# Kernel optimization log

Hardware: AMD Instinct MI355X
Metric: run time of the kernel (lower is better)

Reference implementation:

```python
import jax, jax.numpy as jnp
import numpy as np

B, K, H, W = 16, 32, 28, 28   # batch, set size, image h, image w
HID, OUT = 64, 64             # hid_dim, out_dim
NOPS = 8                      # permutation-equivariant 3->3 pool/broadcast basis ops


def setup_inputs() -> dict:
    key = jax.random.key(0)
    ks = jax.random.split(key, 8)
    def p(k, shape, fan_in):
        return jax.random.normal(k, shape, jnp.float32) / np.float32(np.sqrt(fan_in))
    return dict(
        x=jax.random.normal(ks[0], (B, K, H, W), jnp.float32),
        conv1_w=p(ks[1], (32, 1, 3, 3), 9),
        conv1_b=jnp.zeros((32,), jnp.float32),
        conv2_w=p(ks[2], (64, 32, 3, 3), 32 * 9),
        conv2_b=jnp.zeros((64,), jnp.float32),
        fc_w=p(ks[3], (HID, 64 * 7 * 7), 64 * 7 * 7),
        fc_b=jnp.zeros((HID,), jnp.float32),
        eq_w=p(ks[4], (HID, OUT, NOPS), HID * NOPS),
        eq_b=jnp.zeros((OUT,), jnp.float32),
        out_w=p(ks[5], (1, OUT), OUT),
        out_b=jnp.zeros((1,), jnp.float32),
    )


def _conv2d(x, w, b):
    y = jax.lax.conv_general_dilated(x, w, (1, 1), 'SAME',
                                     dimension_numbers=('NCHW', 'OIHW', 'NCHW'))
    return y + b[None, :, None, None]


def _maxpool2(x):
    return jax.lax.reduce_window(x, -jnp.inf, jax.lax.max,
                                 (1, 1, 2, 2), (1, 1, 2, 2), 'VALID')


def _forward(x, conv1_w, conv1_b, conv2_w, conv2_b, fc_w, fc_b, eq_w, eq_b, out_w, out_b):
    # --- BasicConvNet embed: (B*K, 1, H, W) -> (B*K, HID) ---
    x1 = x.reshape(B * K, 1, H, W)
    h1 = _maxpool2(jax.nn.relu(_conv2d(x1, conv1_w, conv1_b)))   # (B*K, 32, 14, 14)
    h2 = _maxpool2(jax.nn.relu(_conv2d(h1, conv2_w, conv2_b)))   # (B*K, 64, 7, 7)
    feat = jax.nn.relu(h2.reshape(B * K, -1) @ fc_w.T + fc_b)    # (B*K, HID)
    x4 = feat.reshape(B, K, HID)

    # --- triple outer product: (B, HID, K, K, K), no contracted index ---
    x5 = jnp.einsum('bid,bjd,bkd->bdijk', x4, x4, x4)

    # --- SetEq3to3: 8 equivariant pool/broadcast basis ops, contracted with eq_w[d,e,o].
    # Contract each pooled tensor with its slice of eq_w BEFORE broadcasting (same math,
    # avoids materializing 8 full (B,d,K,K,K) op tensors). ---
    m_i  = x5.mean(2)           # (B, d, j, k)
    m_j  = x5.mean(3)           # (B, d, i, k)
    m_k  = x5.mean(4)           # (B, d, i, j)
    m_ij = m_i.mean(2)          # (B, d, k)
    m_ik = m_i.mean(3)          # (B, d, j)
    m_jk = m_j.mean(3)          # (B, d, i)
    m_all = m_ij.mean(2)        # (B, d)

    x6 = (jnp.einsum('bdijk,de->beijk', x5, eq_w[:, :, 0])
          + jnp.einsum('bdjk,de->bejk', m_i, eq_w[:, :, 1])[:, :, None, :, :]
          + jnp.einsum('bdik,de->beik', m_j, eq_w[:, :, 2])[:, :, :, None, :]
          + jnp.einsum('bdij,de->beij', m_k, eq_w[:, :, 3])[:, :, :, :, None]
          + jnp.einsum('bdk,de->bek', m_ij, eq_w[:, :, 4])[:, :, None, None, :]
          + jnp.einsum('bdj,de->bej', m_ik, eq_w[:, :, 5])[:, :, None, :, None]
          + jnp.einsum('bdi,de->bei', m_jk, eq_w[:, :, 6])[:, :, :, None, None]
          + jnp.einsum('bd,de->be', m_all, eq_w[:, :, 7])[:, :, None, None, None]
          + eq_b[None, :, None, None, None])          # (B, OUT, K, K, K)

    # permute to channels-last, relu, pool over (i,j,k), relu, final linear
    x7 = jax.nn.relu(x6.transpose(0, 2, 3, 4, 1))     # (B, K, K, K, OUT)
    x8 = x7.mean(axis=(1, 2, 3))                      # (B, OUT)
    x9 = jax.nn.relu(x8)
    # dropout_prob = 0 -> identity
    return x9 @ out_w.T + out_b                       # (B, 1)


def reference(x, conv1_w, conv1_b, conv2_w, conv2_b, fc_w, fc_b, eq_w, eq_b, out_w, out_b):
    return _forward(x, conv1_w, conv1_b, conv2_w, conv2_b, fc_w, fc_b,
                    eq_w, eq_b, out_w, out_b)
```

## Files before the change

kernel.cpp:

```cpp
#include <hip/hip_runtime.h>
#include <hip/hip_bf16.h>


typedef __attribute__((ext_vector_type(8))) short short8;
typedef __attribute__((ext_vector_type(4))) float f32x4;

__device__ __forceinline__ f32x4 mfma_bf16(short8 a, short8 b, f32x4 c) {
  return __builtin_amdgcn_mfma_f32_16x16x32_bf16(a, b, c, 0, 0, 0);
}

__device__ __forceinline__ unsigned short f2bs(float f) {
  unsigned int u = __float_as_uint(f);
  unsigned int r = u + 0x7fffu + ((u >> 16) & 1u);
  return (unsigned short)(r >> 16);
}
__device__ __forceinline__ unsigned int pk2(float x, float y) {
  union { __hip_bfloat162 h; unsigned int u; } cv;
  cv.h = __float22bfloat162_rn(make_float2(x, y));
  return cv.u;
}
__device__ __forceinline__ void ub8(const short* p, float* f) {
  uint4 u = *(const uint4*)p;
  f[0] = __uint_as_float(u.x << 16); f[1] = __uint_as_float(u.x & 0xffff0000u);
  f[2] = __uint_as_float(u.y << 16); f[3] = __uint_as_float(u.y & 0xffff0000u);
  f[4] = __uint_as_float(u.z << 16); f[5] = __uint_as_float(u.z & 0xffff0000u);
  f[6] = __uint_as_float(u.w << 16); f[7] = __uint_as_float(u.w & 0xffff0000u);
}

__global__ __launch_bounds__(256) void k0_prep(const float* __restrict__ eqw,
    const float* __restrict__ w2, const float* __restrict__ fcw,
    float* __restrict__ W7t, short* __restrict__ Wtb,
    short* __restrict__ w2p, short* __restrict__ fcwb) {
  const int b = blockIdx.x, t = threadIdx.x;
  if (b < 8) {
    const int m = b;
    for (int idx = t; idx < 4096; idx += 256) {
      int e = idx >> 6, d = idx & 63;
      float v = eqw[d*512 + e*8 + m];
      if (m == 7) W7t[idx] = v;
      else        Wtb[m*4096 + idx] = (short)f2bs(v);
    }
  } else if (b == 8) {
    for (int idx = t; idx < 18432; idx += 256) {
      int s2 = idx & 7, c = (idx >> 3) & 63, quad = (idx >> 9) & 3, dd = idx >> 11;
      w2p[idx] = (short)f2bs(w2[c*288 + (quad*8 + s2)*9 + dd]);
    }
  } else {
    int base = (b - 9)*12544 + t;
    for (int q = 0; q < 49; ++q) {
      int idx = base + q*256;
      fcwb[idx] = (short)f2bs(fcw[idx]);
    }
  }
}

__global__ __launch_bounds__(256, 2) void kA_conv(const float* __restrict__ x,
    const float* __restrict__ w1, const float* __restrict__ b1,
    const short* __restrict__ w2p, const float* __restrict__ b2,
    const short* __restrict__ fcwb, const float* __restrict__ fcb,
    float* __restrict__ feat) {
  const int n = blockIdx.x, t = threadIdx.x;
  __shared__ float si[30*30];
  __shared__ float sw[32*9];
  __shared__ float sb[32];
  __shared__ __align__(16) short inT[16*18*40];
  __shared__ __align__(16) float h2f[3136];
  __shared__ float sf4[256];
  const int wv = t >> 6, l = t & 63, quad = l >> 4, col = l & 15;

  const int c_out = wv*16 + col;
  short8 Bq[9];
  {
    const short8* wp = (const short8*)w2p + quad*64 + c_out;
#pragma unroll
    for (int dd = 0; dd < 9; ++dd) Bq[dd] = wp[dd*256];
  }
  const float bb2 = b2[c_out];

  for (int idx = t; idx < 900; idx += 256) si[idx] = 0.f;
  {
    unsigned int* zp = (unsigned int*)inT;
    for (int idx = t; idx < 5760; idx += 256) zp[idx] = 0u;
  }
  for (int idx = t; idx < 288; idx += 256) sw[idx] = w1[idx];
  if (t < 32) sb[t] = b1[t];
  __syncthreads();
  for (int idx = t; idx < 784; idx += 256) {
    int y = idx / 28, xx = idx - y*28;
    si[(y+1)*30 + xx + 1] = x[n*784 + idx];
  }
  __syncthreads();

  {
    const int cg = t & 7;
    float wreg[4][9], breg[4];
#pragma unroll
    for (int cc = 0; cc < 4; ++cc) {
      breg[cc] = sb[cg*4 + cc];
#pragma unroll
      for (int q = 0; q < 9; ++q) wreg[cc][q] = sw[(cg*4 + cc)*9 + q];
    }
    for (int idx = t; idx < 1568; idx += 256) {
      int pos = idx >> 3;
      int py = pos / 14, px = pos - py*14;
      float pt[4][4];
#pragma unroll
      for (int r = 0; r < 4; ++r)
#pragma unroll
        for (int q = 0; q < 4; ++q)
          pt[r][q] = si[(2*py + r)*30 + 2*px + q];
      float res[4];
#pragma unroll
      for (int cc = 0; cc < 4; ++cc) {
        float best = 0.f;
#pragma unroll
        for (int a = 0; a < 2; ++a)
#pragma unroll
          for (int b3 = 0; b3 < 2; ++b3) {
            float v = breg[cc]
              + wreg[cc][0]*pt[a+0][b3+0] + wreg[cc][1]*pt[a+0][b3+1] + wreg[cc][2]*pt[a+0][b3+2]
              + wreg[cc][3]*pt[a+1][b3+0] + wreg[cc][4]*pt[a+1][b3+1] + wreg[cc][5]*pt[a+1][b3+2]
              + wreg[cc][6]*pt[a+2][b3+0] + wreg[cc][7]*pt[a+2][b3+1] + wreg[cc][8]*pt[a+2][b3+2];
            best = fmaxf(best, v);
          }
        res[cc] = best;
      }
      uint2 pkd;
      pkd.x = pk2(res[0], res[1]);
      pkd.y = pk2(res[2], res[3]);
      *(uint2*)&inT[(py+1)*720 + (px+1)*40 + cg*4] = pkd;
    }
  }
  __syncthreads();

  for (int p = 0; p < 7; ++p) {
    short8 Ar[4][3];
#pragma unroll
    for (int rr = 0; rr < 4; ++rr)
#pragma unroll
      for (int dx = 0; dx < 3; ++dx)
        Ar[rr][dx] = *(const short8*)&inT[(2*p + rr)*720 + (col + dx)*40 + quad*8];
    f32x4 a0 = {0.f,0.f,0.f,0.f}, a1 = {0.f,0.f,0.f,0.f};
#pragma unroll
    for (int dy = 0; dy < 3; ++dy)
#pragma unroll
      for (int dx = 0; dx < 3; ++dx) {
        a0 = mfma_bf16(Ar[dy][dx],     Bq[dy*3 + dx], a0);
        a1 = mfma_bf16(Ar[dy + 1][dx], Bq[dy*3 + dx], a1);
      }
#pragma unroll
    for (int a = 0; a < 2; ++a) {
      int px = quad*2 + a;
      if (px < 7) {
        float m0 = fmaxf(fmaxf(a0[2*a], a0[2*a + 1]), fmaxf(a1[2*a], a1[2*a + 1]));
        h2f[c_out*49 + p*7 + px] = fmaxf(m0 + bb2, 0.f);
      }
    }
  }
  {
    const short* Wrow = fcwb + l*3136 + wv*784;
    const float* Hrow = h2f + wv*784;
    float a0 = 0.f, a1 = 0.f, a2 = 0.f, a3 = 0.f;
#pragma unroll 7
    for (int j = 0; j < 98; ++j) {
      float wf[8]; ub8(&Wrow[j*8], wf);
      float4 hx = *(const float4*)&Hrow[j*8];
      float4 hy = *(const float4*)&Hrow[j*8 + 4];
      a0 += wf[0]*hx.x + wf[4]*hy.x;
      a1 += wf[1]*hx.y + wf[5]*hy.y;
      a2 += wf[2]*hx.z + wf[6]*hy.z;
      a3 += wf[3]*hx.w + wf[7]*hy.w;
    }
    sf4[wv*64 + l] = (a0 + a1) + (a2 + a3);
  }
  __syncthreads();
  if (t < 64) {
    float v = sf4[t] + sf4[64 + t] + sf4[128 + t] + sf4[192 + t] + fcb[t];
    feat[n*64 + t] = fmaxf(v, 0.f);
  }
}

__global__ __launch_bounds__(256) void k5_mfma(const float* __restrict__ feat,
    const short* __restrict__ Wtb, const float* __restrict__ W7t,
    const float* __restrict__ eqb, float* __restrict__ x8p) {
  __shared__ __align__(16) float Fm[32*68];
  __shared__ __align__(16) float FI[64];
  __shared__ __align__(16) float SV[64];
  __shared__ __align__(16) float SC[64];
  __shared__ __align__(16) float TC[64];
  __shared__ __align__(16) float C0[64];
  __shared__ float C0P[128];
  __shared__ float KCf[32*68];
  __shared__ float JCf[32*68];
  __shared__ float RED[256];
  __shared__ __align__(16) short Fb[32*72];
  __shared__ __align__(16) short QPb[64*72];
  __shared__ __align__(16) short G2b[64*72];
  __shared__ __align__(16) short G3b[64*72];

  const int i = blockIdx.x, b = blockIdx.y, t = threadIdx.x;
  const int w = t >> 6, l = t & 63, quad = l >> 4, col = l & 15;

  for (int idx = t; idx < 2048; idx += 256) {
    int r = idx >> 6, d = idx & 63;
    float v = feat[b*2048 + idx];
    Fm[r*68 + d] = v;
    Fb[r*72 + d] = (short)f2bs(v);
  }
  if (t < 64) FI[t] = feat[b*2048 + i*64 + t];
  __syncthreads();

  if (t < 64) {
    float a = 0.f;
#pragma unroll
    for (int r = 0; r < 32; ++r) a += Fm[r*68 + t];
    a *= (1.f/32.f);
    SV[t] = a;
    SC[t] = a*a*a;
  }
  __syncthreads();

  if (t < 64) {
    const float* W7 = W7t + t*64;
    float acc = 0.f;
#pragma unroll
    for (int d = 0; d < 64; d += 4) {
      float4 w4 = *(const float4*)&W7[d];
      acc += SC[d]*w4.x + SC[d+1]*w4.y + SC[d+2]*w4.z + SC[d+3]*w4.w;
    }
    TC[t] = acc + eqb[t];
  }

  {
    const int e = t >> 2, dbase = (t & 3) * 16;
#pragma unroll
    for (int h = 0; h < 2; ++h) {
      int off = dbase + h*8;
      float w0[8], w1r[8], w2r[8], w3r[8], w4r[8], w5r[8];
      ub8(&Wtb[0*4096 + e*64 + off], w0);
      ub8(&Wtb[1*4096 + e*64 + off], w1r);
      ub8(&Wtb[2*4096 + e*64 + off], w2r);
      ub8(&Wtb[3*4096 + e*64 + off], w3r);
      ub8(&Wtb[4*4096 + e*64 + off], w4r);
      ub8(&Wtb[5*4096 + e*64 + off], w5r);
      uint4 qv, g2v, g3v;
      unsigned int* qp = &qv.x;
      unsigned int* g2p = &g2v.x;
      unsigned int* g3p = &g3v.x;
#pragma unroll
      for (int j = 0; j < 4; ++j) {
        float fi0 = FI[off + 2*j],     fi1 = FI[off + 2*j + 1];
        float s0  = SV[off + 2*j],     s1  = SV[off + 2*j + 1];
        float q0 = fi0*w0[2*j]   + s0*w1r[2*j];
        float q1 = fi1*w0[2*j+1] + s1*w1r[2*j+1];
        float a0 = s0*(fi0*w2r[2*j]   + s0*w4r[2*j]);
        float a1 = s1*(fi1*w2r[2*j+1] + s1*w4r[2*j+1]);
        float c0 = s0*(fi0*w3r[2*j]   + s0*w5r[2*j]);
        float c1 = s1*(fi1*w3r[2*j+1] + s1*w5r[2*j+1]);
        qp[j]  = pk2(q0, q1);
        g2p[j] = pk2(a0, a1);
        g3p[j] = pk2(c0, c1);
      }
      *(uint4*)&QPb[e*72 + off] = qv;
      *(uint4*)&G2b[e*72 + off] = g2v;
      *(uint4*)&G3b[e*72 + off] = g3v;
    }
  }
  if (t < 128) {
    int e = t & 63, dh = t >> 6;
    const short* W6 = Wtb + 6*4096 + e*64 + dh*32;
    float a = 0.f;
#pragma unroll
    for (int g = 0; g < 4; ++g) {
      float wf[8];
      ub8(&W6[g*8], wf);
#pragma unroll
      for (int dd = 0; dd < 8; ++dd) {
        int d = dh*32 + g*8 + dd;
        float sd = SV[d];
        a += sd*sd*FI[d]*wf[dd];
      }
    }
    C0P[dh*64 + e] = a;
  }
  __syncthreads();

  if (w < 2) {
    const short* G = w ? G3b : G2b;
    float* DST = w ? JCf : KCf;
    short8 Bf[4][2];
#pragma unroll
    for (int n = 0; n < 4; ++n)
#pragma unroll
      for (int s2 = 0; s2 < 2; ++s2)
        Bf[n][s2] = *(const short8*)&G[(n*16 + col)*72 + s2*32 + quad*8];
#pragma unroll
    for (int m = 0; m < 2; ++m) {
      short8 A0 = *(const short8*)&Fb[(m*16 + col)*72 + quad*8];
      short8 A1 = *(const short8*)&Fb[(m*16 + col)*72 + 32 + quad*8];
#pragma unroll
      for (int n = 0; n < 4; ++n) {
        f32x4 z = {0.f, 0.f, 0.f, 0.f};
        f32x4 ac = mfma_bf16(A1, Bf[n][1], mfma_bf16(A0, Bf[n][0], z));
#pragma unroll
        for (int r = 0; r < 4; ++r)
          DST[(m*16 + quad*4 + r)*68 + n*16 + col] = ac[r];
      }
    }
  } else if (w == 2) {
    C0[l] = C0P[l] + C0P[64 + l] + TC[l];
  }
  __syncthreads();

  float kcv[2][4][4];
#pragma unroll
  for (int kb2 = 0; kb2 < 2; ++kb2)
#pragma unroll
    for (int r = 0; r < 4; ++r)
#pragma unroll
      for (int n = 0; n < 4; ++n)
        kcv[kb2][r][n] = KCf[(kb2*16 + quad*4 + r)*68 + n*16 + col];
  short8 Bq[4][2];
#pragma unroll
  for (int n = 0; n < 4; ++n)
#pragma unroll
    for (int s2 = 0; s2 < 2; ++s2)
      Bq[n][s2] = *(const short8*)&QPb[(n*16 + col)*72 + s2*32 + quad*8];

  float4 fkv[2][4];
#pragma unroll
  for (int kb2 = 0; kb2 < 2; ++kb2) {
    const float* fk = &Fm[(kb2*16 + col)*68 + quad*8];
    fkv[kb2][0] = *(const float4*)(fk);
    fkv[kb2][1] = *(const float4*)(fk + 4);
    fkv[kb2][2] = *(const float4*)(fk + 32);
    fkv[kb2][3] = *(const float4*)(fk + 36);
  }

  float sum[4] = {0.f, 0.f, 0.f, 0.f};
  union SU { short8 v; unsigned int u[4]; };

#pragma unroll
  for (int jj = 0; jj < 8; ++jj) {
    float jcq[4];
#pragma unroll
    for (int n = 0; n < 4; ++n)
      jcq[n] = JCf[(w*8 + jj)*68 + n*16 + col] + C0[n*16 + col];
    const float* fj = &Fm[(w*8 + jj)*68 + quad*8];
    float4 j0 = *(const float4*)(fj);
    float4 j1 = *(const float4*)(fj + 4);
    float4 j2 = *(const float4*)(fj + 32);
    float4 j3 = *(const float4*)(fj + 36);
#pragma unroll
    for (int kb2 = 0; kb2 < 2; ++kb2) {
      float4 k0 = fkv[kb2][0], k1 = fkv[kb2][1];
      float4 k2v = fkv[kb2][2], k3v = fkv[kb2][3];
      SU A0, A1;
      A0.u[0] = pk2(j0.x*k0.x, j0.y*k0.y);
      A0.u[1] = pk2(j0.z*k0.z, j0.w*k0.w);
      A0.u[2] = pk2(j1.x*k1.x, j1.y*k1.y);
      A0.u[3] = pk2(j1.z*k1.z, j1.w*k1.w);
      A1.u[0] = pk2(j2.x*k2v.x, j2.y*k2v.y);
      A1.u[1] = pk2(j2.z*k2v.z, j2.w*k2v.w);
      A1.u[2] = pk2(j3.x*k3v.x, j3.y*k3v.y);
      A1.u[3] = pk2(j3.z*k3v.z, j3.w*k3v.w);
      f32x4 ac[4];
#pragma unroll
      for (int n = 0; n < 4; ++n) {
        f32x4 z = {0.f, 0.f, 0.f, 0.f};
        ac[n] = mfma_bf16(A1.v, Bq[n][1], mfma_bf16(A0.v, Bq[n][0], z));
      }
#pragma unroll
      for (int n = 0; n < 4; ++n)
#pragma unroll
        for (int r = 0; r < 4; ++r) {
          float v = ac[n][r] + kcv[kb2][r][n] + jcq[n];
          sum[n] += fmaxf(v, 0.f);
        }
    }
  }

#pragma unroll
  for (int n = 0; n < 4; ++n) {
    float v = sum[n];
    v += __shfl_xor(v, 16, 64);
    v += __shfl_xor(v, 32, 64);
    if (l < 16) RED[w*64 + n*16 + l] = v;
  }
  __syncthreads();
  if (t < 64) {
    float tot = RED[t] + RED[64 + t] + RED[128 + t] + RED[192 + t];
    x8p[(b*32 + i)*64 + t] = tot;
  }
}

__global__ __launch_bounds__(64) void k6_out(const float* __restrict__ x8p,
    const float* __restrict__ ow, const float* __restrict__ ob,
    float* __restrict__ out) {
  const int bb = blockIdx.x, t = threadIdx.x;
  float a = 0.f;
#pragma unroll
  for (int i = 0; i < 32; ++i) a += x8p[(bb*32 + i)*64 + t];
  float v = fmaxf(a * (1.f/32768.f), 0.f) * ow[t];
#pragma unroll
  for (int off = 32; off > 0; off >>= 1) v += __shfl_down(v, off, 64);
  if (t == 0) out[bb] = v + ob[0];
}

extern "C" void kernel_launch(void* const* d_in, const int* in_sizes, int n_in,
                              void* d_out, int out_size, void* d_ws, size_t ws_size,
                              hipStream_t stream) {
  const float* x   = (const float*)d_in[0];
  const float* c1w = (const float*)d_in[1];
  const float* c1b = (const float*)d_in[2];
  const float* c2w = (const float*)d_in[3];
  const float* c2b = (const float*)d_in[4];
  const float* fcw = (const float*)d_in[5];
  const float* fcb = (const float*)d_in[6];
  const float* eqw = (const float*)d_in[7];
  const float* eqb = (const float*)d_in[8];
  const float* ow  = (const float*)d_in[9];
  const float* ob  = (const float*)d_in[10];
  float* out = (float*)d_out;

  float* feat = (float*)d_ws;
  float* x8p  = feat + 32768;
  float* W7t  = x8p + 32768;
  short* Wtb  = (short*)(W7t + 4096);
  short* w2p  = Wtb + 28672;
  short* fcwb = w2p + 18432;
  (void)in_sizes; (void)n_in; (void)out_size; (void)ws_size;

  hipLaunchKernelGGL(k0_prep, dim3(25), dim3(256), 0, stream,
                     eqw, c2w, fcw, W7t, Wtb, w2p, fcwb);
  hipLaunchKernelGGL(kA_conv, dim3(512), dim3(256), 0, stream,
                     x, c1w, c1b, w2p, c2b, fcwb, fcb, feat);
  hipLaunchKernelGGL(k5_mfma, dim3(32, 16), dim3(256), 0, stream,
                     feat, Wtb, W7t, eqb, x8p);
  hipLaunchKernelGGL(k6_out,  dim3(16),  dim3(64),  0, stream, x8p, ow, ob, out);
}
```

Before: 136.5 us.

## Fold weight prep kernel into conv kernel and read fp32 weights directly

Removes the separate k0_prep launch. The eq_w repacking now runs in 8 extra blocks appended to the conv grid. Conv2 weights are converted to bf16 per thread in registers, and the FC weights are read directly as fp32 instead of a pre-converted bf16 copy. This saves a kernel launch and a serialization point, but doubles FC weight read traffic and adds 72 float registers of per-thread conversion work, which may raise register pressure.

```diff
diff --git a/kernel.cpp b/kernel.cpp
--- a/kernel.cpp
+++ b/kernel.cpp
@@ -27,39 +27,23 @@
   f[6] = __uint_as_float(u.w << 16); f[7] = __uint_as_float(u.w & 0xffff0000u);
 }
 
-__global__ __launch_bounds__(256) void k0_prep(const float* __restrict__ eqw,
-    const float* __restrict__ w2, const float* __restrict__ fcw,
-    float* __restrict__ W7t, short* __restrict__ Wtb,
-    short* __restrict__ w2p, short* __restrict__ fcwb) {
-  const int b = blockIdx.x, t = threadIdx.x;
-  if (b < 8) {
-    const int m = b;
+__global__ __launch_bounds__(256, 2) void kA_conv(const float* __restrict__ x,
+    const float* __restrict__ w1, const float* __restrict__ b1,
+    const float* __restrict__ w2, const float* __restrict__ b2,
+    const float* __restrict__ fcw, const float* __restrict__ fcb,
+    const float* __restrict__ eqw, float* __restrict__ W7t, short* __restrict__ Wtb,
+    float* __restrict__ feat) {
+  const int n = blockIdx.x, t = threadIdx.x;
+  if (n >= 512) {
+    const int m = n - 512;
     for (int idx = t; idx < 4096; idx += 256) {
       int e = idx >> 6, d = idx & 63;
       float v = eqw[d*512 + e*8 + m];
       if (m == 7) W7t[idx] = v;
       else        Wtb[m*4096 + idx] = (short)f2bs(v);
     }
-  } else if (b == 8) {
-    for (int idx = t; idx < 18432; idx += 256) {
-      int s2 = idx & 7, c = (idx >> 3) & 63, quad = (idx >> 9) & 3, dd = idx >> 11;
-      w2p[idx] = (short)f2bs(w2[c*288 + (quad*8 + s2)*9 + dd]);
-    }
-  } else {
-    int base = (b - 9)*12544 + t;
-    for (int q = 0; q < 49; ++q) {
-      int idx = base + q*256;
-      fcwb[idx] = (short)f2bs(fcw[idx]);
-    }
-  }
-}
-
-__global__ __launch_bounds__(256, 2) void kA_conv(const float* __restrict__ x,
-    const float* __restrict__ w1, const float* __restrict__ b1,
-    const short* __restrict__ w2p, const float* __restrict__ b2,
-    const short* __restrict__ fcwb, const float* __restrict__ fcb,
-    float* __restrict__ feat) {
-  const int n = blockIdx.x, t = threadIdx.x;
+    return;
+  }
   __shared__ float si[30*30];
   __shared__ float sw[32*9];
   __shared__ float sb[32];
@@ -69,11 +53,24 @@
   const int wv = t >> 6, l = t & 63, quad = l >> 4, col = l & 15;
 
   const int c_out = wv*16 + col;
+  float w72[72];
+  {
+    const float4* src = (const float4*)(w2 + c_out*288 + quad*72);
+#pragma unroll
+    for (int q = 0; q < 18; ++q) {
+      float4 v = src[q];
+      w72[q*4+0] = v.x; w72[q*4+1] = v.y; w72[q*4+2] = v.z; w72[q*4+3] = v.w;
+    }
+  }
+  union SU { short8 v; unsigned int u[4]; };
   short8 Bq[9];
-  {
-    const short8* wp = (const short8*)w2p + quad*64 + c_out;
-#pragma unroll
-    for (int dd = 0; dd < 9; ++dd) Bq[dd] = wp[dd*256];
+#pragma unroll
+  for (int dd = 0; dd < 9; ++dd) {
+    SU b;
+#pragma unroll
+    for (int q = 0; q < 4; ++q)
+      b.u[q] = pk2(w72[(2*q)*9 + dd], w72[(2*q+1)*9 + dd]);
+    Bq[dd] = b.v;
   }
   const float bb2 = b2[c_out];
 
@@ -158,18 +155,19 @@
     }
   }
   {
-    const short* Wrow = fcwb + l*3136 + wv*784;
+    const float* Wrow = fcw + l*3136 + wv*784;
     const float* Hrow = h2f + wv*784;
     float a0 = 0.f, a1 = 0.f, a2 = 0.f, a3 = 0.f;
 #pragma unroll 7
     for (int j = 0; j < 98; ++j) {
-      float wf[8]; ub8(&Wrow[j*8], wf);
+      float4 wa = *(const float4*)&Wrow[j*8];
+      float4 wb = *(const float4*)&Wrow[j*8 + 4];
       float4 hx = *(const float4*)&Hrow[j*8];
       float4 hy = *(const float4*)&Hrow[j*8 + 4];
-      a0 += wf[0]*hx.x + wf[4]*hy.x;
-      a1 += wf[1]*hx.y + wf[5]*hy.y;
-      a2 += wf[2]*hx.z + wf[6]*hy.z;
-      a3 += wf[3]*hx.w + wf[7]*hy.w;
+      a0 += wa.x*hx.x + wb.x*hy.x;
+      a1 += wa.y*hx.y + wb.y*hy.y;
+      a2 += wa.z*hx.z + wb.z*hy.z;
+      a3 += wa.w*hx.w + wb.w*hy.w;
     }
     sf4[wv*64 + l] = (a0 + a1) + (a2 + a3);
   }
@@ -427,14 +425,10 @@
   float* x8p  = feat + 32768;
   float* W7t  = x8p + 32768;
   short* Wtb  = (short*)(W7t + 4096);
-  short* w2p  = Wtb + 28672;
-  short* fcwb = w2p + 18432;
   (void)in_sizes; (void)n_in; (void)out_size; (void)ws_size;
 
-  hipLaunchKernelGGL(k0_prep, dim3(25), dim3(256), 0, stream,
-                     eqw, c2w, fcw, W7t, Wtb, w2p, fcwb);
-  hipLaunchKernelGGL(kA_conv, dim3(512), dim3(256), 0, stream,
-                     x, c1w, c1b, w2p, c2b, fcwb, fcb, feat);
+  hipLaunchKernelGGL(kA_conv, dim3(520), dim3(256), 0, stream,
+                     x, c1w, c1b, c2w, c2b, fcw, fcb, eqw, W7t, Wtb, feat);
   hipLaunchKernelGGL(k5_mfma, dim3(32, 16), dim3(256), 0, stream,
                      feat, Wtb, W7t, eqb, x8p);
   hipLaunchKernelGGL(k6_out,  dim3(16),  dim3(64),  0, stream, x8p, ow, ob, out);
```

Result: slower. 158.6 us (+16.2%).
